# Performance work log

Measured on AMD Instinct MI355X. Metric: run time of the kernel, lower is better.

## Reference

```python
import jax, jax.numpy as jnp
from jax import lax
import numpy as np

N, K, F, H, NG, T = 32768, 16, 64, 128, 1024, 2


def setup_inputs() -> dict:
    key = jax.random.key(0)
    ks = jax.random.split(key, 24)
    def rn(k, shape, s=0.05):
        return jax.random.normal(k, shape, jnp.float32) * s
    inp = {
        'n': jax.random.normal(ks[0], (N, F), jnp.float32),
        'nbr': jax.random.randint(ks[1], (N, K), 0, N),
        # deterministic sorted graph ids -> every graph non-empty (safe segment_max)
        'gid': (jnp.arange(N) * NG) // N,
        'G': NG,
        # SAGEConv layer 1: LSTM(F,F), fc_self/fc_neigh F->H
        'lstm1_Wih': rn(ks[2], (F, 4 * F)), 'lstm1_Whh': rn(ks[3], (F, 4 * F)), 'lstm1_b': jnp.zeros((4 * F,), jnp.float32),
        'fcs1_W': rn(ks[4], (F, H)), 'fcs1_b': jnp.zeros((H,), jnp.float32),
        'fcn1_W': rn(ks[5], (F, H)), 'fcn1_b': jnp.zeros((H,), jnp.float32),
        # SAGEConv layer 2: LSTM(H,H), fc_self/fc_neigh H->H
        'lstm2_Wih': rn(ks[6], (H, 4 * H)), 'lstm2_Whh': rn(ks[7], (H, 4 * H)), 'lstm2_b': jnp.zeros((4 * H,), jnp.float32),
        'fcs2_W': rn(ks[8], (H, H)), 'fcs2_b': jnp.zeros((H,), jnp.float32),
        'fcn2_W': rn(ks[9], (H, H)), 'fcn2_b': jnp.zeros((H,), jnp.float32),
        # WeightedSumAndMax atom weighting: H->1
        'rw_W': rn(ks[10], (H, 1)), 'rw_b': jnp.zeros((1,), jnp.float32),
        # task head: 2H->H, H->T
        'h1_W': rn(ks[11], (2 * H, H)), 'h1_b': jnp.zeros((H,), jnp.float32),
        'h2_W': rn(ks[12], (H, T)), 'h2_b': jnp.zeros((T,), jnp.float32),
    }
    return inp


def _lstm_last(xseq, Wih, Whh, b):
    # xseq: [N, K, Fin]; returns last hidden state [N, Hh]
    Hh = Whh.shape[0]
    h0 = jnp.zeros((xseq.shape[0], Hh), xseq.dtype)
    def step(carry, xt):
        h, c = carry
        g = xt @ Wih + h @ Whh + b  # [N, 4H], torch gate order i,f,g,o
        i, f, gg, o = jnp.split(g, 4, axis=-1)
        c = jax.nn.sigmoid(f) * c + jax.nn.sigmoid(i) * jnp.tanh(gg)
        h = jax.nn.sigmoid(o) * jnp.tanh(c)
        return (h, c), None
    (h, _), _ = lax.scan(step, (h0, h0), jnp.swapaxes(xseq, 0, 1))
    return h


def _sage_layer(x, nbr, Wih, Whh, b, Ws, bs, Wn, bn):
    hn = _lstm_last(x[nbr], Wih, Whh, b)          # LSTM aggregate of neighbors
    return jax.nn.sigmoid(x @ Ws + bs + hn @ Wn + bn)


def reference(n, nbr, gid, G,
              lstm1_Wih, lstm1_Whh, lstm1_b, fcs1_W, fcs1_b, fcn1_W, fcn1_b,
              lstm2_Wih, lstm2_Whh, lstm2_b, fcs2_W, fcs2_b, fcn2_W, fcn2_b,
              rw_W, rw_b, h1_W, h1_b, h2_W, h2_b):
    G = int(G)
    h1 = _sage_layer(n, nbr, lstm1_Wih, lstm1_Whh, lstm1_b, fcs1_W, fcs1_b, fcn1_W, fcn1_b)
    h2 = _sage_layer(h1, nbr, lstm2_Wih, lstm2_Whh, lstm2_b, fcs2_W, fcs2_b, fcn2_W, fcn2_b)
    # WeightedSumAndMax readout
    w = jax.nn.sigmoid(h2 @ rw_W + rw_b)                       # [N,1]
    wsum = jax.ops.segment_sum(w * h2, gid, num_segments=G)    # [G,H]
    mx = jax.ops.segment_max(h2, gid, num_segments=G)          # [G,H]
    gemb = jnp.concatenate([wsum, mx], axis=-1)                # [G,2H]
    y = jax.nn.sigmoid(gemb @ h1_W + h1_b)
    y = jax.nn.sigmoid(y @ h2_W + h2_b)                        # classification
    return y
```

## Files before the change

### kernel.cpp

```cpp
#include <hip/hip_runtime.h>

typedef unsigned short u16;
typedef __attribute__((ext_vector_type(8))) short bf16x8;
typedef __attribute__((ext_vector_type(4))) float f32x4;
typedef __attribute__((ext_vector_type(2))) float f32x2;

constexpr int N_ = 32768;
constexpr int H_ = 128;
constexpr int G_ = 1024;
constexpr int T_ = 2;

__device__ __forceinline__ float sigf(float x){
  float e = __builtin_amdgcn_exp2f(x * -1.44269504f);
  return __builtin_amdgcn_rcpf(1.0f + e);
}
__device__ __forceinline__ f32x2 sig2(f32x2 x){
  f32x2 t = x * -1.44269504f;
  f32x2 e; e.x = __builtin_amdgcn_exp2f(t.x); e.y = __builtin_amdgcn_exp2f(t.y);
  f32x2 d = e + 1.0f;
  float r = __builtin_amdgcn_rcpf(d.x * d.y);
  return (f32x2){r * d.y, r * d.x};
}
__device__ __forceinline__ f32x2 tanh2(f32x2 x){
  f32x2 t = x * 2.88539008f;
  f32x2 e; e.x = __builtin_amdgcn_exp2f(t.x); e.y = __builtin_amdgcn_exp2f(t.y);
  f32x2 d = e + 1.0f;
  float r = __builtin_amdgcn_rcpf(d.x * d.y);
  f32x2 rr = (f32x2){r * d.y, r * d.x};
  return 1.0f - 2.0f*rr;
}
__device__ __forceinline__ u16 f2bf(float f){
  unsigned u = __float_as_uint(f);
  unsigned r = (u + 0x7FFFu + ((u>>16)&1u))>>16;
  return (u16)r;
}
__device__ __forceinline__ unsigned cvt_pk_bf16(float a, float b){
  unsigned r;
  asm("v_cvt_pk_bf16_f32 %0, %1, %2" : "=v"(r) : "v"(a), "v"(b));
  return r;
}
__device__ __forceinline__ float bf2f(u16 h){ return __uint_as_float(((unsigned)h)<<16); }
__device__ __forceinline__ float asf(unsigned u){ return __uint_as_float(u); }
__device__ __forceinline__ f32x4 mfma16(bf16x8 a, bf16x8 b, f32x4 c){
  return __builtin_amdgcn_mfma_f32_16x16x32_bf16(a,b,c,0,0,0);
}

__global__ __launch_bounds__(64)
void pack_all(const float* __restrict__ l1Wih, const float* __restrict__ fcs1W,
              const float* __restrict__ l1Whh, const float* __restrict__ fcn1W,
              const float* __restrict__ l2Wih, const float* __restrict__ fcs2W,
              const float* __restrict__ l2Whh, const float* __restrict__ fcn2W,
              const float* __restrict__ l1b, const float* __restrict__ bs1,
              const float* __restrict__ bn1,
              const float* __restrict__ l2b, const float* __restrict__ bs2,
              const float* __restrict__ bn2,
              u16* BY1, u16* BW1, u16* BN1, u16* BY2, u16* BW2, u16* BN2,
              u16* bY1, u16* bY2)
{
  int b = blockIdx.x;
  const int lane = threadIdx.x;
  if (b == 416) {
    for (int i = lane; i < 1024; i += 64) {
      if (i < 384) {
        int p = i; float v;
        if (p < 256) { int o = (p&3)*64 + ((p>>6)<<4) + ((p>>2)&15); v = l1b[o]; }
        else         { int j = p-256; v = bs1[j] + bn1[j]; }
        bY1[p] = f2bf(v);
      } else {
        int p = i - 384; float v;
        if (p < 512) { int o = (p&3)*128 + ((p>>6)<<4) + ((p>>2)&15); v = l2b[o]; }
        else         { int j = p-512; v = bs2[j] + bn2[j]; }
        bY2[p] = f2bf(v);
      }
    }
    return;
  }
  const float* src; u16* dst; int srcNC, NTtot, ntOff, ntCnt, Fh, perm;
  if      (b < 32)  { src=l1Wih; dst=BY1; srcNC=256; NTtot=24; ntOff=0;  ntCnt=16; Fh=64;  perm=2; }
  else if (b < 48)  { src=fcs1W; dst=BY1; srcNC=128; NTtot=24; ntOff=16; ntCnt=8;  Fh=0;   perm=0; b-=32; }
  else if (b < 80)  { src=l1Whh; dst=BW1; srcNC=256; NTtot=16; ntOff=0;  ntCnt=16; Fh=64;  perm=1; b-=48; }
  else if (b < 96)  { src=fcn1W; dst=BN1; srcNC=128; NTtot=8;  ntOff=0;  ntCnt=8;  Fh=0;   perm=0; b-=80; }
  else if (b < 224) { src=l2Wih; dst=BY2; srcNC=512; NTtot=40; ntOff=0;  ntCnt=32; Fh=128; perm=2; b-=96; }
  else if (b < 256) { src=fcs2W; dst=BY2; srcNC=128; NTtot=40; ntOff=32; ntCnt=8;  Fh=0;   perm=0; b-=224; }
  else if (b < 384) { src=l2Whh; dst=BW2; srcNC=512; NTtot=32; ntOff=0;  ntCnt=32; Fh=128; perm=1; b-=256; }
  else              { src=fcn2W; dst=BN2; srcNC=128; NTtot=8;  ntOff=0;  ntCnt=8;  Fh=0;   perm=0; b-=384; }
  const int ntl = b % ntCnt, kt = b / ntCnt;
  const int n = lane & 15, qq = lane >> 4;
  int pr = ntl*16 + n;
  int o;
  if (perm == 1)      o = ((pr>>4)&3)*Fh + ((pr>>6)<<4) + (pr&15);
  else if (perm == 2) o = (pr&3)*Fh + ((pr>>6)<<4) + ((pr>>2)&15);
  else                o = pr;
  u16* d = dst + ((size_t)((kt*NTtot + ntOff + ntl)*64 + lane))*8;
#pragma unroll
  for (int j = 0; j < 8; ++j) {
    int k = kt*32 + qq*8 + j;
    d[j] = f2bf(src[(size_t)k*srcNC + o]);
  }
}

template<int KT, int NTT, int AF32>
__global__ __launch_bounds__(256, 2)
void gemm_kernel(const void* __restrict__ Ain,
                 const u16* __restrict__ Bpk,
                 const u16* __restrict__ biasbf,
                 u16* __restrict__ out, int out_stride)
{
  constexpr int KA  = KT*32;
  constexpr int NTW = NTT/4;
  constexpr int STR = KA + 8;
  __shared__ __align__(16) u16 a_lds[32*STR];
  const int tid  = threadIdx.x;
  const int base = blockIdx.x*32;
  {
    const int sub = tid & 7, rowl = tid >> 3;
    if constexpr (AF32) {
      const float* src = (const float*)Ain + (size_t)(base+rowl)*KA;
#pragma unroll
      for (int cc = 0; cc < KA/32; ++cc) {
        int e0 = (cc*8+sub)*4;
        float4 v = *(const float4*)(src + e0);
        ushort4 bv;
        bv.x = f2bf(v.x); bv.y = f2bf(v.y); bv.z = f2bf(v.z); bv.w = f2bf(v.w);
        *(ushort4*)(void*)(a_lds + rowl*STR + e0) = bv;
      }
    } else {
      const u16* src = (const u16*)Ain + (size_t)(base+rowl)*KA;
#pragma unroll
      for (int cc = 0; cc < KA/64; ++cc) {
        int e0 = (cc*8+sub)*8;
        uint4 v = *(const uint4*)(const void*)(src + e0);
        *(uint4*)(void*)(a_lds + rowl*STR + e0) = v;
      }
    }
  }
  __syncthreads();
  const int lane = tid & 63, w = tid >> 6;
  const int lc = lane & 15, q = lane >> 4;
  f32x4 acc[2][NTW];
  f32x4 z = {0.f,0.f,0.f,0.f};
#pragma unroll
  for (int m = 0; m < 2; ++m)
#pragma unroll
    for (int j = 0; j < NTW; ++j) acc[m][j] = z;
#pragma unroll
  for (int kt = 0; kt < KT; ++kt) {
    bf16x8 af0 = *(const bf16x8*)(const void*)(a_lds + lc*STR      + kt*32 + q*8);
    bf16x8 af1 = *(const bf16x8*)(const void*)(a_lds + (lc+16)*STR + kt*32 + q*8);
#pragma unroll
    for (int j = 0; j < NTW; ++j) {
      bf16x8 bf = *(const bf16x8*)(const void*)(Bpk + ((size_t)((kt*NTT + w*NTW + j)*64 + lane))*8);
      acc[0][j] = mfma16(af0, bf, acc[0][j]);
      acc[1][j] = mfma16(af1, bf, acc[1][j]);
    }
  }
#pragma unroll
  for (int m = 0; m < 2; ++m)
#pragma unroll
    for (int j = 0; j < NTW; ++j) {
      int col = (w*NTW + j)*16 + lc;
#pragma unroll
      for (int r = 0; r < 4; ++r) {
        int row = base + m*16 + q*4 + r;
        out[(size_t)row*out_stride + col] = f2bf(acc[m][j][r] + bf2f(biasbf[col]));
      }
    }
}

template<int KT, int MT, int MW>
__global__ __launch_bounds__(KT*128, MW)
void lstm_kernel(const int* __restrict__ nbr,
                 const u16* __restrict__ Y, int nctot,
                 const u16* __restrict__ Bpk,
                 const u16* __restrict__ BN,
                 const u16* __restrict__ Sp, int s_stride, int s_coloff,
                 u16* __restrict__ out)
{
  constexpr int F   = KT*32;
  constexpr int NW  = KT*2;
  constexpr int NTT = KT*8;
  constexpr int STR = F + 8;
  constexpr int M   = MT*16;
  __shared__ __align__(16) u16 h_lds[2][M*STR];
  __shared__ int nbr_s[M*16];
  const int tid  = threadIdx.x;
  const int base = blockIdx.x * M;
  const int lane = tid & 63, w = tid >> 6;
  const int lc = lane & 15, q = lane >> 4;

  for (int i = tid; i < M*16; i += NW*64) nbr_s[i] = nbr[base*16 + i];

  bf16x8 bfr[KT][4];
#pragma unroll
  for (int kt = 0; kt < KT; ++kt)
#pragma unroll
    for (int g = 0; g < 4; ++g)
      bfr[kt][g] = *(const bf16x8*)(const void*)(Bpk + ((size_t)((kt*NTT + w*4 + g)*64 + lane))*8);

  f32x2 cs[MT][2];
#pragma unroll
  for (int m = 0; m < MT; ++m)
#pragma unroll
    for (int rp = 0; rp < 2; ++rp) cs[m][rp] = (f32x2){0.f, 0.f};
  __syncthreads();

  const char* Yb = (const char*)Y;
  const unsigned rowbytes = (unsigned)nctot * 2u;
  const unsigned lanebyte = (unsigned)(w*64 + lc*4) * 2u;
  const int wcol = w*16 + lc;

  uint2 yv[MT][4];
#pragma unroll
  for (int m = 0; m < MT; ++m)
#pragma unroll
    for (int r = 0; r < 4; ++r) {
      unsigned vr = (unsigned)nbr_s[(m*16 + q*4 + r)*16];
      yv[m][r] = *(const uint2*)(const void*)(Yb + (vr*rowbytes + lanebyte));
    }

  for (int t = 0; t < 16; ++t) {
    const u16* hr = h_lds[t & 1];
    u16*       hw = h_lds[(t & 1) ^ 1];
#pragma unroll
    for (int m = 0; m < MT; ++m) {
      f32x4 acc[4];
#pragma unroll
      for (int r = 0; r < 4; ++r) {
        acc[0][r] = asf(yv[m][r].x << 16);
        acc[1][r] = asf(yv[m][r].x & 0xffff0000u);
        acc[2][r] = asf(yv[m][r].y << 16);
        acc[3][r] = asf(yv[m][r].y & 0xffff0000u);
      }
      if (t != 0) {
#pragma unroll
        for (int kt = 0; kt < KT; ++kt) {
          bf16x8 af = *(const bf16x8*)(const void*)(hr + (lc + m*16)*STR + kt*32 + q*8);
#pragma unroll
          for (int g = 0; g < 4; ++g) acc[g] = mfma16(af, bfr[kt][g], acc[g]);
        }
      }
#pragma unroll
      for (int rp = 0; rp < 2; ++rp) {
        f32x2 gi = (f32x2){acc[0][2*rp], acc[0][2*rp+1]};
        f32x2 gf = (f32x2){acc[1][2*rp], acc[1][2*rp+1]};
        f32x2 gg = (f32x2){acc[2][2*rp], acc[2][2*rp+1]};
        f32x2 go = (f32x2){acc[3][2*rp], acc[3][2*rp+1]};
        f32x2 c  = sig2(gf)*cs[m][rp] + sig2(gi)*tanh2(gg);
        cs[m][rp] = c;
        f32x2 hh = sig2(go)*tanh2(c);
        unsigned pkd = cvt_pk_bf16(hh.x, hh.y);
        int r0 = m*16 + q*4 + 2*rp;
        hw[r0*STR + wcol]     = (u16)pkd;
        hw[(r0+1)*STR + wcol] = (u16)(pkd >> 16);
      }
    }
    if (t < 15) {
#pragma unroll
      for (int m = 0; m < MT; ++m)
#pragma unroll
        for (int r = 0; r < 4; ++r) {
          unsigned vr = (unsigned)nbr_s[(m*16 + q*4 + r)*16 + t + 1];
          yv[m][r] = *(const uint2*)(const void*)(Yb + (vr*rowbytes + lanebyte));
        }
    }
    __syncthreads();
  }

  constexpr int CPW = 8 / NW;
  const u16* hf = h_lds[0];
#pragma unroll
  for (int cc2 = 0; cc2 < CPW; ++cc2) {
    const int nt = w*CPW + cc2;
    f32x4 a2[MT];
    f32x4 z = {0.f,0.f,0.f,0.f};
#pragma unroll
    for (int m = 0; m < MT; ++m) a2[m] = z;
#pragma unroll
    for (int kt = 0; kt < KT; ++kt) {
      bf16x8 nf = *(const bf16x8*)(const void*)(BN + ((size_t)((kt*8 + nt)*64 + lane))*8);
#pragma unroll
      for (int m = 0; m < MT; ++m) {
        bf16x8 af = *(const bf16x8*)(const void*)(hf + (lc + m*16)*STR + kt*32 + q*8);
        a2[m] = mfma16(af, nf, a2[m]);
      }
    }
    const int col = nt*16 + lc;
#pragma unroll
    for (int m = 0; m < MT; ++m)
#pragma unroll
      for (int r = 0; r < 4; ++r) {
        int row = base + m*16 + q*4 + r;
        float v = a2[m][r] + bf2f(Sp[(size_t)row*s_stride + s_coloff + col]);
        out[(size_t)row*H_ + col] = f2bf(sigf(v));
      }
  }
}

__global__ __launch_bounds__(128)
void head_kernel(const u16* __restrict__ h2, const float* __restrict__ rwW,
                 const float* __restrict__ rwb,
                 const float* __restrict__ h1W, const float* __restrict__ h1b,
                 const float* __restrict__ h2W, const float* __restrict__ h2b,
                 float* __restrict__ out)
{
  __shared__ float h2s[32*H_];
  __shared__ float part[32*4];
  __shared__ float wv[32];
  __shared__ float gemb[2*H_];
  __shared__ float y1[H_];
  const int g = blockIdx.x, t = threadIdx.x;
  for (int r = 0; r < 32; ++r)
    h2s[r*H_ + t] = bf2f(h2[(size_t)(g*32 + r)*H_ + t]);
  __syncthreads();
  { int r = t>>2, qq = t&3; float p = 0.f;
    for (int h = qq*32; h < qq*32+32; ++h) p += h2s[r*H_+h]*rwW[h];
    part[r*4+qq] = p; }
  __syncthreads();
  if (t < 32) wv[t] = sigf(part[t*4]+part[t*4+1]+part[t*4+2]+part[t*4+3]+rwb[0]);
  __syncthreads();
  { float wsum=0.f, mx=-3.402823466e38f;
    for (int r = 0; r < 32; ++r) { float v = h2s[r*H_+t]; wsum += wv[r]*v; mx = fmaxf(mx,v); }
    gemb[t]=wsum; gemb[H_+t]=mx; }
  __syncthreads();
  { float a = h1b[t];
    for (int k = 0; k < 2*H_; ++k) a += gemb[k]*h1W[k*H_+t];
    y1[t]=sigf(a); }
  __syncthreads();
  if (t < T_) {
    float a = h2b[t];
    for (int h = 0; h < H_; ++h) a += y1[h]*h2W[h*T_+t];
    out[(size_t)g*T_+t] = sigf(a);
  }
}

extern "C" void kernel_launch(void* const* d_in, const int* in_sizes, int n_in,
                              void* d_out, int out_size, void* d_ws, size_t ws_size,
                              hipStream_t stream) {
  const float* n_feat = (const float*)d_in[0];
  const int*   nbr    = (const int*)d_in[1];
  const float* l1Wih = (const float*)d_in[4];
  const float* l1Whh = (const float*)d_in[5];
  const float* l1b   = (const float*)d_in[6];
  const float* fcs1W = (const float*)d_in[7];
  const float* fcs1b = (const float*)d_in[8];
  const float* fcn1W = (const float*)d_in[9];
  const float* fcn1b = (const float*)d_in[10];
  const float* l2Wih = (const float*)d_in[11];
  const float* l2Whh = (const float*)d_in[12];
  const float* l2b   = (const float*)d_in[13];
  const float* fcs2W = (const float*)d_in[14];
  const float* fcs2b = (const float*)d_in[15];
  const float* fcn2W = (const float*)d_in[16];
  const float* fcn2b = (const float*)d_in[17];
  const float* rwW   = (const float*)d_in[18];
  const float* rwb   = (const float*)d_in[19];
  const float* h1W   = (const float*)d_in[20];
  const float* h1b   = (const float*)d_in[21];
  const float* h2W   = (const float*)d_in[22];
  const float* h2b   = (const float*)d_in[23];

  char* ws = (char*)d_ws;
  u16* Y   = (u16*)(ws);
  u16* h1  = (u16*)(ws + 41943040);
  u16* h2  = (u16*)(ws + 50331648);
  char* wt = ws + 58720256;
  u16* BY1 = (u16*)(wt);
  u16* BW1 = (u16*)(wt + 49152);
  u16* BN1 = (u16*)(wt + 81920);
  u16* BY2 = (u16*)(wt + 98304);
  u16* BW2 = (u16*)(wt + 262144);
  u16* BN2 = (u16*)(wt + 393216);
  u16* bY1 = (u16*)(wt + 425984);
  u16* bY2 = (u16*)(wt + 426752);

  pack_all<<<417, 64, 0, stream>>>(l1Wih, fcs1W, l1Whh, fcn1W,
                                   l2Wih, fcs2W, l2Whh, fcn2W,
                                   l1b, fcs1b, fcn1b, l2b, fcs2b, fcn2b,
                                   BY1, BW1, BN1, BY2, BW2, BN2, bY1, bY2);

  gemm_kernel<2,24,1><<<1024, 256, 0, stream>>>(n_feat, BY1, bY1, Y, 384);
  lstm_kernel<2,1,6><<<2048, 256, 0, stream>>>(nbr, Y, 384, BW1, BN1, Y, 384, 256, h1);

  gemm_kernel<4,40,0><<<1024, 256, 0, stream>>>(h1, BY2, bY2, Y, 640);
  lstm_kernel<4,1,4><<<2048, 512, 0, stream>>>(nbr, Y, 640, BW2, BN2, Y, 640, 512, h2);

  head_kernel<<<G_, 128, 0, stream>>>(h2, rwW, rwb, h1W, h1b, h2W, h2b, (float*)d_out);
}
```

Before: 309.0 us.

## Fuse layer-1 LSTM with layer-2 input GEMM and prescale gate weights

Adds a fused kernel that runs the layer-1 LSTM aggregation, the fc_neigh sigmoid, and the layer-2 input projection (Wih|fcs2) in one pass. This skips writing h1 to global memory and launching a separate GEMM. Gate weights and biases are also pre-multiplied by -log2(e) or 2*log2(e) at pack time, so the per-step sigmoid/tanh drops a multiply. The fused path runs only when the workspace is large enough, with a fallback to the old pipeline. Folding the scale into weights before the bf16 rounding slightly changes numerics.

```diff
diff --git a/kernel.cpp b/kernel.cpp
--- a/kernel.cpp
+++ b/kernel.cpp
@@ -14,12 +14,18 @@
   float e = __builtin_amdgcn_exp2f(x * -1.44269504f);
   return __builtin_amdgcn_rcpf(1.0f + e);
 }
-__device__ __forceinline__ f32x2 sig2(f32x2 x){
-  f32x2 t = x * -1.44269504f;
-  f32x2 e; e.x = __builtin_amdgcn_exp2f(t.x); e.y = __builtin_amdgcn_exp2f(t.y);
+__device__ __forceinline__ f32x2 sig2p(f32x2 xp){
+  f32x2 e; e.x = __builtin_amdgcn_exp2f(xp.x); e.y = __builtin_amdgcn_exp2f(xp.y);
   f32x2 d = e + 1.0f;
   float r = __builtin_amdgcn_rcpf(d.x * d.y);
   return (f32x2){r * d.y, r * d.x};
+}
+__device__ __forceinline__ f32x2 tanh2p(f32x2 xp){
+  f32x2 e; e.x = __builtin_amdgcn_exp2f(xp.x); e.y = __builtin_amdgcn_exp2f(xp.y);
+  f32x2 d = e + 1.0f;
+  float r = __builtin_amdgcn_rcpf(d.x * d.y);
+  f32x2 rr = (f32x2){r * d.y, r * d.x};
+  return 1.0f - 2.0f*rr;
 }
 __device__ __forceinline__ f32x2 tanh2(f32x2 x){
   f32x2 t = x * 2.88539008f;
@@ -63,13 +69,19 @@
     for (int i = lane; i < 1024; i += 64) {
       if (i < 384) {
         int p = i; float v;
-        if (p < 256) { int o = (p&3)*64 + ((p>>6)<<4) + ((p>>2)&15); v = l1b[o]; }
-        else         { int j = p-256; v = bs1[j] + bn1[j]; }
+        if (p < 256) {
+          int o = (p&3)*64 + ((p>>6)<<4) + ((p>>2)&15);
+          float sc = ((p&3)==2) ? 2.88539008f : -1.44269504f;
+          v = l1b[o]*sc;
+        } else { int j = p-256; v = bs1[j] + bn1[j]; }
         bY1[p] = f2bf(v);
       } else {
         int p = i - 384; float v;
-        if (p < 512) { int o = (p&3)*128 + ((p>>6)<<4) + ((p>>2)&15); v = l2b[o]; }
-        else         { int j = p-512; v = bs2[j] + bn2[j]; }
+        if (p < 512) {
+          int o = (p&3)*128 + ((p>>6)<<4) + ((p>>2)&15);
+          float sc = ((p&3)==2) ? 2.88539008f : -1.44269504f;
+          v = l2b[o]*sc;
+        } else { int j = p-512; v = bs2[j] + bn2[j]; }
         bY2[p] = f2bf(v);
       }
     }
@@ -87,15 +99,21 @@
   const int ntl = b % ntCnt, kt = b / ntCnt;
   const int n = lane & 15, qq = lane >> 4;
   int pr = ntl*16 + n;
-  int o;
-  if (perm == 1)      o = ((pr>>4)&3)*Fh + ((pr>>6)<<4) + (pr&15);
-  else if (perm == 2) o = (pr&3)*Fh + ((pr>>6)<<4) + ((pr>>2)&15);
-  else                o = pr;
+  int o; float scale = 1.0f;
+  if (perm == 1) {
+    int g = (pr>>4)&3;
+    o = g*Fh + ((pr>>6)<<4) + (pr&15);
+    scale = (g==2) ? 2.88539008f : -1.44269504f;
+  } else if (perm == 2) {
+    int g = pr&3;
+    o = g*Fh + ((pr>>6)<<4) + ((pr>>2)&15);
+    scale = (g==2) ? 2.88539008f : -1.44269504f;
+  } else o = pr;
   u16* d = dst + ((size_t)((kt*NTtot + ntOff + ntl)*64 + lane))*8;
 #pragma unroll
   for (int j = 0; j < 8; ++j) {
     int k = kt*32 + qq*8 + j;
-    d[j] = f2bf(src[(size_t)k*srcNC + o]);
+    d[j] = f2bf(src[(size_t)k*srcNC + o] * scale);
   }
 }
 
@@ -245,9 +263,9 @@
         f32x2 gf = (f32x2){acc[1][2*rp], acc[1][2*rp+1]};
         f32x2 gg = (f32x2){acc[2][2*rp], acc[2][2*rp+1]};
         f32x2 go = (f32x2){acc[3][2*rp], acc[3][2*rp+1]};
-        f32x2 c  = sig2(gf)*cs[m][rp] + sig2(gi)*tanh2(gg);
+        f32x2 c  = sig2p(gf)*cs[m][rp] + sig2p(gi)*tanh2p(gg);
         cs[m][rp] = c;
-        f32x2 hh = sig2(go)*tanh2(c);
+        f32x2 hh = sig2p(go)*tanh2(c);
         unsigned pkd = cvt_pk_bf16(hh.x, hh.y);
         int r0 = m*16 + q*4 + 2*rp;
         hw[r0*STR + wcol]     = (u16)pkd;
@@ -293,6 +311,132 @@
         float v = a2[m][r] + bf2f(Sp[(size_t)row*s_stride + s_coloff + col]);
         out[(size_t)row*H_ + col] = f2bf(sigf(v));
       }
+  }
+}
+
+__global__ __launch_bounds__(256, 6)
+void lstm1_y2(const int* __restrict__ nbr,
+              const u16* __restrict__ Y1,
+              const u16* __restrict__ Bpk,
+              const u16* __restrict__ BN,
+              const u16* __restrict__ BY2,
+              const u16* __restrict__ bY2,
+              u16* __restrict__ Y2)
+{
+  constexpr int STR = 72;
+  __shared__ __align__(16) u16 h_lds[2][16*STR];
+  __shared__ __align__(16) u16 hs[16*136];
+  __shared__ int nbr_s[256];
+  const int tid  = threadIdx.x;
+  const int base = blockIdx.x * 16;
+  const int lane = tid & 63, w = tid >> 6;
+  const int lc = lane & 15, q = lane >> 4;
+
+  nbr_s[tid] = nbr[base*16 + tid];
+
+  bf16x8 bfr[2][4];
+#pragma unroll
+  for (int kt = 0; kt < 2; ++kt)
+#pragma unroll
+    for (int g = 0; g < 4; ++g)
+      bfr[kt][g] = *(const bf16x8*)(const void*)(Bpk + ((size_t)((kt*16 + w*4 + g)*64 + lane))*8);
+
+  f32x2 cs[2];
+  cs[0] = (f32x2){0.f,0.f}; cs[1] = (f32x2){0.f,0.f};
+  __syncthreads();
+
+  const char* Yb = (const char*)Y1;
+  const unsigned lanebyte = (unsigned)(w*64 + lc*4) * 2u;
+  const int wcol = w*16 + lc;
+
+  uint2 yv[4];
+#pragma unroll
+  for (int r = 0; r < 4; ++r) {
+    unsigned vr = (unsigned)nbr_s[(q*4 + r)*16];
+    yv[r] = *(const uint2*)(const void*)(Yb + (vr*768u + lanebyte));
+  }
+
+  for (int t = 0; t < 16; ++t) {
+    const u16* hr = h_lds[t & 1];
+    u16*       hw = h_lds[(t & 1) ^ 1];
+    f32x4 acc[4];
+#pragma unroll
+    for (int r = 0; r < 4; ++r) {
+      acc[0][r] = asf(yv[r].x << 16);
+      acc[1][r] = asf(yv[r].x & 0xffff0000u);
+      acc[2][r] = asf(yv[r].y << 16);
+      acc[3][r] = asf(yv[r].y & 0xffff0000u);
+    }
+    if (t != 0) {
+#pragma unroll
+      for (int kt = 0; kt < 2; ++kt) {
+        bf16x8 af = *(const bf16x8*)(const void*)(hr + lc*STR + kt*32 + q*8);
+#pragma unroll
+        for (int g = 0; g < 4; ++g) acc[g] = mfma16(af, bfr[kt][g], acc[g]);
+      }
+    }
+#pragma unroll
+    for (int rp = 0; rp < 2; ++rp) {
+      f32x2 gi = (f32x2){acc[0][2*rp], acc[0][2*rp+1]};
+      f32x2 gf = (f32x2){acc[1][2*rp], acc[1][2*rp+1]};
+      f32x2 gg = (f32x2){acc[2][2*rp], acc[2][2*rp+1]};
+      f32x2 go = (f32x2){acc[3][2*rp], acc[3][2*rp+1]};
+      f32x2 c  = sig2p(gf)*cs[rp] + sig2p(gi)*tanh2p(gg);
+      cs[rp] = c;
+      f32x2 hh = sig2p(go)*tanh2(c);
+      unsigned pkd = cvt_pk_bf16(hh.x, hh.y);
+      int r0 = q*4 + 2*rp;
+      hw[r0*STR + wcol]     = (u16)pkd;
+      hw[(r0+1)*STR + wcol] = (u16)(pkd >> 16);
+    }
+    if (t < 15) {
+#pragma unroll
+      for (int r = 0; r < 4; ++r) {
+        unsigned vr = (unsigned)nbr_s[(q*4 + r)*16 + t + 1];
+        yv[r] = *(const uint2*)(const void*)(Yb + (vr*768u + lanebyte));
+      }
+    }
+    __syncthreads();
+  }
+
+  const u16* hf = h_lds[0];
+#pragma unroll
+  for (int cc2 = 0; cc2 < 2; ++cc2) {
+    const int nt = w*2 + cc2;
+    f32x4 a2 = {0.f,0.f,0.f,0.f};
+#pragma unroll
+    for (int kt = 0; kt < 2; ++kt) {
+      bf16x8 nf = *(const bf16x8*)(const void*)(BN + ((size_t)((kt*8 + nt)*64 + lane))*8);
+      bf16x8 af = *(const bf16x8*)(const void*)(hf + lc*STR + kt*32 + q*8);
+      a2 = mfma16(af, nf, a2);
+    }
+    const int col = nt*16 + lc;
+#pragma unroll
+    for (int r = 0; r < 4; ++r) {
+      int row = base + q*4 + r;
+      float v = a2[r] + bf2f(Y1[(size_t)row*384 + 256 + col]);
+      hs[(q*4 + r)*136 + col] = f2bf(sigf(v));
+    }
+  }
+  __syncthreads();
+
+#pragma unroll
+  for (int j = 0; j < 10; ++j) {
+    const int nt = w*10 + j;
+    const int col = nt*16 + lc;
+    float bv = bf2f(bY2[col]);
+    f32x4 acc;
+#pragma unroll
+    for (int r = 0; r < 4; ++r) acc[r] = bv;
+#pragma unroll
+    for (int kt = 0; kt < 4; ++kt) {
+      bf16x8 af = *(const bf16x8*)(const void*)(hs + lc*136 + kt*32 + q*8);
+      bf16x8 bf = *(const bf16x8*)(const void*)(BY2 + ((size_t)((kt*40 + nt)*64 + lane))*8);
+      acc = mfma16(af, bf, acc);
+    }
+#pragma unroll
+    for (int r = 0; r < 4; ++r)
+      Y2[(size_t)(base + q*4 + r)*640 + col] = f2bf(acc[r]);
   }
 }
 
@@ -360,29 +504,51 @@
   const float* h2b   = (const float*)d_in[23];
 
   char* ws = (char*)d_ws;
-  u16* Y   = (u16*)(ws);
-  u16* h1  = (u16*)(ws + 41943040);
-  u16* h2  = (u16*)(ws + 50331648);
-  char* wt = ws + 58720256;
-  u16* BY1 = (u16*)(wt);
-  u16* BW1 = (u16*)(wt + 49152);
-  u16* BN1 = (u16*)(wt + 81920);
-  u16* BY2 = (u16*)(wt + 98304);
-  u16* BW2 = (u16*)(wt + 262144);
-  u16* BN2 = (u16*)(wt + 393216);
-  u16* bY1 = (u16*)(wt + 425984);
-  u16* bY2 = (u16*)(wt + 426752);
-
-  pack_all<<<417, 64, 0, stream>>>(l1Wih, fcs1W, l1Whh, fcn1W,
-                                   l2Wih, fcs2W, l2Whh, fcn2W,
-                                   l1b, fcs1b, fcn1b, l2b, fcs2b, fcn2b,
-                                   BY1, BW1, BN1, BY2, BW2, BN2, bY1, bY2);
-
-  gemm_kernel<2,24,1><<<1024, 256, 0, stream>>>(n_feat, BY1, bY1, Y, 384);
-  lstm_kernel<2,1,6><<<2048, 256, 0, stream>>>(nbr, Y, 384, BW1, BN1, Y, 384, 256, h1);
-
-  gemm_kernel<4,40,0><<<1024, 256, 0, stream>>>(h1, BY2, bY2, Y, 640);
-  lstm_kernel<4,1,4><<<2048, 512, 0, stream>>>(nbr, Y, 640, BW2, BN2, Y, 640, 512, h2);
-
-  head_kernel<<<G_, 128, 0, stream>>>(h2, rwW, rwb, h1W, h1b, h2W, h2b, (float*)d_out);
-}
+
+  if (ws_size >= 67600000) {
+    u16* Y1 = (u16*)(ws);
+    u16* Y2 = (u16*)(ws + 25165824);
+    u16* h2 = (u16*)(ws);
+    char* wt = ws + 67108864;
+    u16* BY1 = (u16*)(wt);
+    u16* BW1 = (u16*)(wt + 49152);
+    u16* BN1 = (u16*)(wt + 81920);
+    u16* BY2 = (u16*)(wt + 98304);
+    u16* BW2 = (u16*)(wt + 262144);
+    u16* BN2 = (u16*)(wt + 393216);
+    u16* bY1 = (u16*)(wt + 425984);
+    u16* bY2 = (u16*)(wt + 426752);
+
+    pack_all<<<417, 64, 0, stream>>>(l1Wih, fcs1W, l1Whh, fcn1W,
+                                     l2Wih, fcs2W, l2Whh, fcn2W,
+                                     l1b, fcs1b, fcn1b, l2b, fcs2b, fcn2b,
+                                     BY1, BW1, BN1, BY2, BW2, BN2, bY1, bY2);
+    gemm_kernel<2,24,1><<<1024, 256, 0, stream>>>(n_feat, BY1, bY1, Y1, 384);
+    lstm1_y2<<<2048, 256, 0, stream>>>(nbr, Y1, BW1, BN1, BY2, bY2, Y2);
+    lstm_kernel<4,1,4><<<2048, 512, 0, stream>>>(nbr, Y2, 640, BW2, BN2, Y2, 640, 512, h2);
+    head_kernel<<<G_, 128, 0, stream>>>(h2, rwW, rwb, h1W, h1b, h2W, h2b, (float*)d_out);
+  } else {
+    u16* Y   = (u16*)(ws);
+    u16* h1  = (u16*)(ws + 41943040);
+    u16* h2  = (u16*)(ws + 50331648);
+    char* wt = ws + 58720256;
+    u16* BY1 = (u16*)(wt);
+    u16* BW1 = (u16*)(wt + 49152);
+    u16* BN1 = (u16*)(wt + 81920);
+    u16* BY2 = (u16*)(wt + 98304);
+    u16* BW2 = (u16*)(wt + 262144);
+    u16* BN2 = (u16*)(wt + 393216);
+    u16* bY1 = (u16*)(wt + 425984);
+    u16* bY2 = (u16*)(wt + 426752);
+
+    pack_all<<<417, 64, 0, stream>>>(l1Wih, fcs1W, l1Whh, fcn1W,
+                                     l2Wih, fcs2W, l2Whh, fcn2W,
+                                     l1b, fcs1b, fcn1b, l2b, fcs2b, fcn2b,
+                                     BY1, BW1, BN1, BY2, BW2, BN2, bY1, bY2);
+    gemm_kernel<2,24,1><<<1024, 256, 0, stream>>>(n_feat, BY1, bY1, Y, 384);
+    lstm_kernel<2,1,6><<<2048, 256, 0, stream>>>(nbr, Y, 384, BW1, BN1, Y, 384, 256, h1);
+    gemm_kernel<4,40,0><<<1024, 256, 0, stream>>>(h1, BY2, bY2, Y, 640);
+    lstm_kernel<4,1,4><<<2048, 512, 0, stream>>>(nbr, Y, 640, BW2, BN2, Y, 640, 512, h2);
+    head_kernel<<<G_, 128, 0, stream>>>(h2, rwW, rwb, h1W, h1b, h2W, h2b, (float*)d_out);
+  }
+}
```

Result: faster. 280.5 us (-9.2%).
